# Kernel tuning notes

Measured on AMD Instinct MI355X. Metric: run time of the kernel, lower is better.

The kernel has to match this reference:

```python
import jax, jax.numpy as jnp
import numpy as np

IN, OUT, FP, B, S = 8192, 28672, 128, 32, 1


def setup_inputs() -> dict:
    key = jax.random.key(0)
    k = jax.random.split(key, 6)
    x = jax.random.normal(k[0], (B, S, IN), dtype=jnp.float32).astype(jnp.float16)
    # int8 quantized weight, stored as [OUT, IN]
    weight = jax.random.randint(k[1], (OUT, IN), -128, 128, dtype=jnp.int32).astype(jnp.int8)
    # per-output-column dequant scale (fp16, positive, small)
    scale_col = (jax.random.uniform(k[2], (1, OUT), dtype=jnp.float32) * 0.01 + 1e-4).astype(jnp.float16)
    # fp16 cache of the outlier weight columns [OUT, FP]
    weight_cache = (jax.random.normal(k[3], (OUT, FP), dtype=jnp.float32) * 0.02).astype(jnp.float16)
    bias = (jax.random.normal(k[4], (OUT,), dtype=jnp.float32) * 0.02).astype(jnp.float16)
    # sorted unique outlier column indices
    ind = jnp.sort(jax.random.permutation(k[5], IN)[:FP]).astype(jnp.int32)
    return {"x": x, "weight": weight, "scale_col": scale_col,
            "weight_cache": weight_cache, "bias": bias, "ind": ind}


def reference(x, weight, scale_col, weight_cache, bias, ind):
    out_features = weight.shape[0]
    shape = x.shape[:-1] + (out_features,)
    inputs = x.reshape(-1, x.shape[-1])                       # [M, IN] fp16
    # ExtractOutliersAndSetToZeros: gather outlier activation columns, zero them
    act_outliers = inputs[:, ind]                              # [M, FP] fp16
    tmp = inputs.at[:, ind].set(jnp.float16(0))                # [M, IN]
    # FindRowScale (bit=8): symmetric per-row int8 scale
    x_scale = jnp.max(jnp.abs(tmp), axis=1, keepdims=True) / jnp.float16(127)  # [M, 1]
    q_x = jnp.clip(jnp.round(tmp / x_scale), -128, 127).astype(jnp.int8)       # [M, IN]
    # int8FusedDequantize: int8 GEMM -> dequant with row/col scales -> add fp16 outlier GEMM
    y_int = jnp.matmul(q_x.astype(jnp.int32), weight.T.astype(jnp.int32))      # [M, OUT] int32
    y = y_int.astype(jnp.float16) * x_scale * scale_col                        # dequantize
    y = y + jnp.matmul(act_outliers, weight_cache.T)                           # outlier fp16 GEMM
    y = y + bias
    return y.reshape(shape)
```

## Files before the change

kernel.cpp:

```cpp
#include <hip/hip_runtime.h>
#include <hip/hip_fp16.h>

#define IN_F   8192
#define OUT_F  28672
#define NFP    128
#define NB     32
#define KQTOT  (IN_F / 4)

#define WS_QPK 0
#define WS_XS  262144
#define WS_ACT 263168

#if __has_builtin(__builtin_amdgcn_sdot4)
__device__ __forceinline__ int dot4(int a, int b, int c) {
    return __builtin_amdgcn_sdot4(a, b, c, false);
}
#else
__device__ __forceinline__ int dot4(int a, int b, int c) {
    #pragma unroll
    for (int j = 0; j < 4; j++)
        c += ((a << (24 - 8 * j)) >> 24) * ((b << (24 - 8 * j)) >> 24);
    return c;
}
#endif

__device__ __forceinline__ int pack8(int4 v) {
    return (v.x & 0xFF) | ((v.y & 0xFF) << 8) | ((v.z & 0xFF) << 16) | (v.w << 24);
}

__global__ __launch_bounds__(256) void quant_kernel(
    const float* __restrict__ x, const int* __restrict__ ind,
    int* __restrict__ q_pk, float* __restrict__ xs_out,
    float* __restrict__ act_out)
{
    __shared__ unsigned char flags[IN_F];
    __shared__ float redbuf[4];
    __shared__ float xs_sh;
    const int tid = threadIdx.x;
    const int b = blockIdx.x;

    int* fl4 = (int*)flags;
    for (int i = tid; i < IN_F / 4; i += 256) fl4[i] = 0;
    __syncthreads();
    if (tid < NFP) flags[ind[tid]] = 1;
    __syncthreads();

    const float* xrow = x + (size_t)b * IN_F;
    const float4* x4 = (const float4*)xrow;
    float mx = 0.f;
    for (int c = tid; c < IN_F / 4; c += 256) {
        float4 v = x4[c];
        int fw = fl4[c];
        if (!(fw & 0x000000FF)) mx = fmaxf(mx, fabsf(v.x));
        if (!(fw & 0x0000FF00)) mx = fmaxf(mx, fabsf(v.y));
        if (!(fw & 0x00FF0000)) mx = fmaxf(mx, fabsf(v.z));
        if (!(fw & 0xFF000000)) mx = fmaxf(mx, fabsf(v.w));
    }
    #pragma unroll
    for (int off = 32; off > 0; off >>= 1) {
        float o = __shfl_down(mx, off, 64);
        mx = o > mx ? o : mx;
    }
    if ((tid & 63) == 0) redbuf[tid >> 6] = mx;
    __syncthreads();
    if (tid == 0) {
        float m = redbuf[0];
        #pragma unroll
        for (int i = 1; i < 4; i++) m = redbuf[i] > m ? redbuf[i] : m;
        float xs = __half2float(__float2half_rn(m / 127.0f));
        xs_sh = xs;
        xs_out[b] = xs;
    }
    __syncthreads();
    const float xs = xs_sh;

    for (int c = tid; c < IN_F / 4; c += 256) {
        float4 v = x4[c];
        int fw = fl4[c];
        float ee[4];
        ee[0] = (fw & 0x000000FF) ? 0.f : v.x;
        ee[1] = (fw & 0x0000FF00) ? 0.f : v.y;
        ee[2] = (fw & 0x00FF0000) ? 0.f : v.z;
        ee[3] = (fw & 0xFF000000) ? 0.f : v.w;
        int pk = 0;
        #pragma unroll
        for (int j = 0; j < 4; j++) {
            float qf = __half2float(__float2half_rn(ee[j] / xs));
            float r = rintf(qf);
            r = fminf(fmaxf(r, -128.f), 127.f);
            int qi = (int)r;
            pk |= (qi & 0xFF) << (8 * j);
        }
        q_pk[(size_t)b * KQTOT + c] = pk;
    }
    if (tid < NFP) act_out[b * NFP + tid] = xrow[ind[tid]];
}

#define OT   64
#define KT   128
#define KQ   32
#define WROW 36

__global__ __launch_bounds__(256) void gemm_kernel(
    const int* __restrict__ w, const int* __restrict__ q_pk,
    const float* __restrict__ xs_ws, const float* __restrict__ act_ws,
    const float* __restrict__ sc, const float* __restrict__ wc,
    const float* __restrict__ bias, float* __restrict__ out)
{
    __shared__ int   w_p[OT * WROW] __attribute__((aligned(16)));
    __shared__ int   q_t[NB][KQ]    __attribute__((aligned(16)));
    __shared__ float act_l[NB * NFP];
    __shared__ float xs_l[NB];

    const int tid = threadIdx.x;
    const int o_base = blockIdx.x * OT;

    for (int i = tid; i < NB * NFP; i += 256) act_l[i] = act_ws[i];
    if (tid < NB) xs_l[tid] = xs_ws[tid];

    const int o_lo = tid & 31;
    const int bq = tid >> 5;

    const int st_r = tid >> 2;
    const int st_c = tid & 3;

    const int sq_b = tid >> 3;
    const int sq_c = tid & 7;

    int acc0[4] = {0, 0, 0, 0};
    int acc1[4] = {0, 0, 0, 0};

    for (int k0 = 0; k0 < IN_F; k0 += KT) {
        __syncthreads();
        {
            const int* src = w + (size_t)(o_base + st_r) * IN_F + k0 + st_c * 4;
            int* dst = &w_p[st_r * WROW + st_c];
            #pragma unroll
            for (int i = 0; i < 8; i++) {
                int4 v = *(const int4*)(src + i * 16);
                dst[i * 4] = pack8(v);
            }
        }
        {
            int4 v = *(const int4*)(q_pk + (size_t)sq_b * KQTOT + (k0 >> 2) + sq_c * 4);
            *(int4*)&q_t[sq_b][sq_c * 4] = v;
        }
        __syncthreads();

        const int* wrow0 = &w_p[o_lo * WROW];
        const int* wrow1 = &w_p[(o_lo + 32) * WROW];
        #pragma unroll
        for (int g = 0; g < KQ / 4; g++) {
            int4 w0 = *(const int4*)(wrow0 + g * 4);
            int4 w1 = *(const int4*)(wrow1 + g * 4);
            int4 qv[4];
            #pragma unroll
            for (int bb = 0; bb < 4; bb++)
                qv[bb] = *(const int4*)(&q_t[bq * 4 + bb][g * 4]);
            #pragma unroll
            for (int bb = 0; bb < 4; bb++) {
                acc0[bb] = dot4(w0.x, qv[bb].x, acc0[bb]);
                acc0[bb] = dot4(w0.y, qv[bb].y, acc0[bb]);
                acc0[bb] = dot4(w0.z, qv[bb].z, acc0[bb]);
                acc0[bb] = dot4(w0.w, qv[bb].w, acc0[bb]);
                acc1[bb] = dot4(w1.x, qv[bb].x, acc1[bb]);
                acc1[bb] = dot4(w1.y, qv[bb].y, acc1[bb]);
                acc1[bb] = dot4(w1.z, qv[bb].z, acc1[bb]);
                acc1[bb] = dot4(w1.w, qv[bb].w, acc1[bb]);
            }
        }
    }

    const int o0 = o_base + o_lo, o1 = o0 + 32;
    const float sc0 = sc[o0], sc1 = sc[o1];
    const float bi0 = bias[o0], bi1 = bias[o1];
    const float* wc0 = wc + (size_t)o0 * NFP;
    const float* wc1 = wc + (size_t)o1 * NFP;

    float dot0[4] = {0, 0, 0, 0}, dot1[4] = {0, 0, 0, 0};
    for (int j = 0; j < NFP; j += 4) {
        float4 a0 = *(const float4*)(wc0 + j);
        float4 a1 = *(const float4*)(wc1 + j);
        #pragma unroll
        for (int bb = 0; bb < 4; bb++) {
            const float4 av = *(const float4*)(&act_l[(bq * 4 + bb) * NFP + j]);
            dot0[bb] += av.x * a0.x + av.y * a0.y + av.z * a0.z + av.w * a0.w;
            dot1[bb] += av.x * a1.x + av.y * a1.y + av.z * a1.z + av.w * a1.w;
        }
    }

    #pragma unroll
    for (int bb = 0; bb < 4; bb++) {
        const int batch = bq * 4 + bb;
        const float xsv = xs_l[batch];
        out[(size_t)batch * OUT_F + o0] = (float)acc0[bb] * xsv * sc0 + dot0[bb] + bi0;
        out[(size_t)batch * OUT_F + o1] = (float)acc1[bb] * xsv * sc1 + dot1[bb] + bi1;
    }
}

extern "C" void kernel_launch(void* const* d_in, const int* in_sizes, int n_in,
                              void* d_out, int out_size, void* d_ws, size_t ws_size,
                              hipStream_t stream) {
    const float* x    = (const float*)d_in[0];
    const int*   wgt  = (const int*)d_in[1];
    const float* scol = (const float*)d_in[2];
    const float* wch  = (const float*)d_in[3];
    const float* bias = (const float*)d_in[4];
    const int*   ind  = (const int*)d_in[5];
    float* out = (float*)d_out;

    int*   q_pk = (int*)((char*)d_ws + WS_QPK);
    float* xs   = (float*)((char*)d_ws + WS_XS);
    float* act  = (float*)((char*)d_ws + WS_ACT);

    quant_kernel<<<NB, 256, 0, stream>>>(x, ind, q_pk, xs, act);
    gemm_kernel<<<OUT_F / OT, 256, 0, stream>>>(wgt, q_pk, xs, act, scol, wch, bias, out);
}
```

Before: 1.230 ms.

## Use int8 MFMA 32x32x32 instructions for quantized GEMM instead of sdot4

Replaces the per-thread sdot4 accumulation with __builtin_amdgcn_mfma_i32_32x32x32_i8, where each of two waves computes a 32-batch by 32-output tile. The K tile is doubled to 256 and the block shrinks to 128 threads. The outlier fp16 dot product and the epilogue are remapped to the MFMA output layout. The aim is to cut ALU cost in the compute loop, though the kernel stays bound by weight bandwidth, since the weights are stored as int32 per element and packed on load.

```diff
diff --git a/kernel.cpp b/kernel.cpp
--- a/kernel.cpp
+++ b/kernel.cpp
@@ -11,18 +11,8 @@
 #define WS_XS  262144
 #define WS_ACT 263168
 
-#if __has_builtin(__builtin_amdgcn_sdot4)
-__device__ __forceinline__ int dot4(int a, int b, int c) {
-    return __builtin_amdgcn_sdot4(a, b, c, false);
-}
-#else
-__device__ __forceinline__ int dot4(int a, int b, int c) {
-    #pragma unroll
-    for (int j = 0; j < 4; j++)
-        c += ((a << (24 - 8 * j)) >> 24) * ((b << (24 - 8 * j)) >> 24);
-    return c;
-}
-#endif
+typedef int v4i  __attribute__((ext_vector_type(4)));
+typedef int v16i __attribute__((ext_vector_type(16)));
 
 __device__ __forceinline__ int pack8(int4 v) {
     return (v.x & 0xFF) | ((v.y & 0xFF) << 8) | ((v.z & 0xFF) << 16) | (v.w << 24);
@@ -97,104 +87,95 @@
 }
 
 #define OT   64
-#define KT   128
-#define KQ   32
-#define WROW 36
+#define KT   256
+#define KQT  (KT / 4)
+#define WROW 68
+#define QROW 68
 
-__global__ __launch_bounds__(256) void gemm_kernel(
+__global__ __launch_bounds__(128) void gemm_kernel(
     const int* __restrict__ w, const int* __restrict__ q_pk,
     const float* __restrict__ xs_ws, const float* __restrict__ act_ws,
     const float* __restrict__ sc, const float* __restrict__ wc,
     const float* __restrict__ bias, float* __restrict__ out)
 {
     __shared__ int   w_p[OT * WROW] __attribute__((aligned(16)));
-    __shared__ int   q_t[NB][KQ]    __attribute__((aligned(16)));
+    __shared__ int   q_t[NB * QROW] __attribute__((aligned(16)));
     __shared__ float act_l[NB * NFP];
     __shared__ float xs_l[NB];
 
-    const int tid = threadIdx.x;
-    const int o_base = blockIdx.x * OT;
+    const int tid  = threadIdx.x;
+    const int wave = tid >> 6;
+    const int lane = tid & 63;
+    const int nl   = lane & 31;
+    const int half = lane >> 5;
 
-    for (int i = tid; i < NB * NFP; i += 256) act_l[i] = act_ws[i];
+    const int blk_o = blockIdx.x * OT;
+    const int n = blk_o + wave * 32 + nl;
+
+    for (int i = tid; i < NB * NFP; i += 128) act_l[i] = act_ws[i];
     if (tid < NB) xs_l[tid] = xs_ws[tid];
 
-    const int o_lo = tid & 31;
-    const int bq = tid >> 5;
-
-    const int st_r = tid >> 2;
-    const int st_c = tid & 3;
-
-    const int sq_b = tid >> 3;
-    const int sq_c = tid & 7;
-
-    int acc0[4] = {0, 0, 0, 0};
-    int acc1[4] = {0, 0, 0, 0};
+    v16i acc;
+    #pragma unroll
+    for (int r = 0; r < 16; r++) acc[r] = 0;
 
     for (int k0 = 0; k0 < IN_F; k0 += KT) {
         __syncthreads();
-        {
-            const int* src = w + (size_t)(o_base + st_r) * IN_F + k0 + st_c * 4;
-            int* dst = &w_p[st_r * WROW + st_c];
-            #pragma unroll
-            for (int i = 0; i < 8; i++) {
-                int4 v = *(const int4*)(src + i * 16);
-                dst[i * 4] = pack8(v);
-            }
+        #pragma unroll 4
+        for (int i = 0; i < 8; i++) {
+            int u  = i * 128 + tid;
+            int r  = u >> 4;
+            int c4 = u & 15;
+            const int* src = w + (size_t)(blk_o + r) * IN_F + k0 + c4 * 16;
+            int4 a = *(const int4*)(src + 0);
+            int4 b = *(const int4*)(src + 4);
+            int4 c = *(const int4*)(src + 8);
+            int4 d = *(const int4*)(src + 12);
+            int4 pk = make_int4(pack8(a), pack8(b), pack8(c), pack8(d));
+            *(int4*)&w_p[r * WROW + c4 * 4] = pk;
         }
-        {
-            int4 v = *(const int4*)(q_pk + (size_t)sq_b * KQTOT + (k0 >> 2) + sq_c * 4);
-            *(int4*)&q_t[sq_b][sq_c * 4] = v;
+        #pragma unroll
+        for (int i = 0; i < 4; i++) {
+            int u  = i * 128 + tid;
+            int b  = u >> 4;
+            int c4 = u & 15;
+            int4 v = *(const int4*)(q_pk + (size_t)b * KQTOT + (k0 >> 2) + c4 * 4);
+            *(int4*)&q_t[b * QROW + c4 * 4] = v;
         }
         __syncthreads();
 
-        const int* wrow0 = &w_p[o_lo * WROW];
-        const int* wrow1 = &w_p[(o_lo + 32) * WROW];
+        const int* qrow = &q_t[nl * QROW + half * 4];
+        const int* wrow = &w_p[(wave * 32 + nl) * WROW + half * 4];
         #pragma unroll
-        for (int g = 0; g < KQ / 4; g++) {
-            int4 w0 = *(const int4*)(wrow0 + g * 4);
-            int4 w1 = *(const int4*)(wrow1 + g * 4);
-            int4 qv[4];
-            #pragma unroll
-            for (int bb = 0; bb < 4; bb++)
-                qv[bb] = *(const int4*)(&q_t[bq * 4 + bb][g * 4]);
-            #pragma unroll
-            for (int bb = 0; bb < 4; bb++) {
-                acc0[bb] = dot4(w0.x, qv[bb].x, acc0[bb]);
-                acc0[bb] = dot4(w0.y, qv[bb].y, acc0[bb]);
-                acc0[bb] = dot4(w0.z, qv[bb].z, acc0[bb]);
-                acc0[bb] = dot4(w0.w, qv[bb].w, acc0[bb]);
-                acc1[bb] = dot4(w1.x, qv[bb].x, acc1[bb]);
-                acc1[bb] = dot4(w1.y, qv[bb].y, acc1[bb]);
-                acc1[bb] = dot4(w1.z, qv[bb].z, acc1[bb]);
-                acc1[bb] = dot4(w1.w, qv[bb].w, acc1[bb]);
-            }
+        for (int s = 0; s < KT / 32; s++) {
+            v4i a = *(const v4i*)(qrow + s * 8);
+            v4i b = *(const v4i*)(wrow + s * 8);
+            acc = __builtin_amdgcn_mfma_i32_32x32x32_i8(a, b, acc, 0, 0, 0);
         }
     }
 
-    const int o0 = o_base + o_lo, o1 = o0 + 32;
-    const float sc0 = sc[o0], sc1 = sc[o1];
-    const float bi0 = bias[o0], bi1 = bias[o1];
-    const float* wc0 = wc + (size_t)o0 * NFP;
-    const float* wc1 = wc + (size_t)o1 * NFP;
+    const float scn = sc[n];
+    const float bin = bias[n];
+    const float* wcn = wc + (size_t)n * NFP;
 
-    float dot0[4] = {0, 0, 0, 0}, dot1[4] = {0, 0, 0, 0};
+    float dots[16];
+    #pragma unroll
+    for (int r = 0; r < 16; r++) dots[r] = 0.f;
+
     for (int j = 0; j < NFP; j += 4) {
-        float4 a0 = *(const float4*)(wc0 + j);
-        float4 a1 = *(const float4*)(wc1 + j);
+        float4 wv = *(const float4*)(wcn + j);
         #pragma unroll
-        for (int bb = 0; bb < 4; bb++) {
-            const float4 av = *(const float4*)(&act_l[(bq * 4 + bb) * NFP + j]);
-            dot0[bb] += av.x * a0.x + av.y * a0.y + av.z * a0.z + av.w * a0.w;
-            dot1[bb] += av.x * a1.x + av.y * a1.y + av.z * a1.z + av.w * a1.w;
+        for (int r = 0; r < 16; r++) {
+            int b = (r & 3) + 8 * (r >> 2) + 4 * half;
+            float4 av = *(const float4*)(&act_l[b * NFP + j]);
+            dots[r] += av.x * wv.x + av.y * wv.y + av.z * wv.z + av.w * wv.w;
         }
     }
 
     #pragma unroll
-    for (int bb = 0; bb < 4; bb++) {
-        const int batch = bq * 4 + bb;
-        const float xsv = xs_l[batch];
-        out[(size_t)batch * OUT_F + o0] = (float)acc0[bb] * xsv * sc0 + dot0[bb] + bi0;
-        out[(size_t)batch * OUT_F + o1] = (float)acc1[bb] * xsv * sc1 + dot1[bb] + bi1;
+    for (int r = 0; r < 16; r++) {
+        int b = (r & 3) + 8 * (r >> 2) + 4 * half;
+        out[(size_t)b * OUT_F + n] = (float)acc[r] * xs_l[b] * scn + dots[r] + bin;
     }
 }
 
@@ -214,5 +195,5 @@
     float* act  = (float*)((char*)d_ws + WS_ACT);
 
     quant_kernel<<<NB, 256, 0, stream>>>(x, ind, q_pk, xs, act);
-    gemm_kernel<<<OUT_F / OT, 256, 0, stream>>>(wgt, q_pk, xs, act, scol, wch, bias, out);
+    gemm_kernel<<<OUT_F / OT, 128, 0, stream>>>(wgt, q_pk, xs, act, scol, wch, bias, out);
 }
```

Result: faster. 1.186 ms (-3.6%).
